# Kernel optimization log

Measured on AMD Instinct MI355X. Metric: run time of the kernel, lower is better.

The kernel has to match this reference:

```python
import jax, jax.numpy as jnp
import numpy as np

N = 50000   # nodes
E = 800000  # edges
G = 128     # graphs in batch
H = 128     # hidden/out dim
K = 3       # GMM kernels
L = 4       # layers
PD = 2      # pseudo_dim_MoNet
NC = 10     # classes
BN_EPS = 1e-5


def setup_inputs() -> dict:
    key = jax.random.key(0)
    ks = jax.random.split(key, 16)
    s = 1.0 / np.sqrt(H)
    inp = {
        "feature": jax.random.normal(ks[0], (N, H), jnp.float32),
        "edge_index": jax.random.randint(ks[1], (2, E), 0, N, dtype=jnp.int32),
        "batch": jnp.sort(jax.random.randint(ks[2], (N,), 0, G, dtype=jnp.int32)),
        "emb_w": jax.random.normal(ks[3], (H, H), jnp.float32) * s,
        "emb_b": jnp.zeros((H,), jnp.float32),
        "fc_w": jax.random.normal(ks[4], (L, K * H, H), jnp.float32) * s,   # per-layer GMMConv fc (no bias)
        "mu": jax.random.normal(ks[5], (L, K, PD), jnp.float32) * 0.1,
        "inv_sigma": jnp.ones((L, K, PD), jnp.float32),
        "bn_gamma": jnp.ones((L, H), jnp.float32),
        "bn_beta": jnp.zeros((L, H), jnp.float32),
        "pp_w": jax.random.normal(ks[6], (L, PD, 2), jnp.float32) * 0.7,   # pseudo_proj Linear(2, dim)
        "pp_b": jnp.zeros((L, PD), jnp.float32),
        "mlp_w0": jax.random.normal(ks[7], (H // 2, H), jnp.float32) * s,
        "mlp_b0": jnp.zeros((H // 2,), jnp.float32),
        "mlp_w1": jax.random.normal(ks[8], (H // 4, H // 2), jnp.float32) * (1.0 / np.sqrt(H // 2)),
        "mlp_b1": jnp.zeros((H // 4,), jnp.float32),
        "mlp_w2": jax.random.normal(ks[9], (NC, H // 4), jnp.float32) * (1.0 / np.sqrt(H // 4)),
        "mlp_b2": jnp.zeros((NC,), jnp.float32),
    }
    return inp


def _forward(feature, edge_index, batch, emb_w, emb_b, fc_w, mu, inv_sigma,
             bn_gamma, bn_beta, pp_w, pp_b, mlp_w0, mlp_b0, mlp_w1, mlp_b1, mlp_w2, mlp_b2):
    row, col = edge_index[0], edge_index[1]
    h = feature @ emb_w.T + emb_b                                   # [N,H]

    # degree-based pseudo coordinates (per edge)
    ones_e = jnp.ones((E,), jnp.float32)
    deg_r = jax.ops.segment_sum(ones_e, row, num_segments=N)
    deg_c = jax.ops.segment_sum(ones_e, col, num_segments=N)
    srcs = 1.0 / jnp.sqrt(deg_r[row] + 1.0)
    dsts = 1.0 / jnp.sqrt(deg_c[col] + 1.0)
    pseudo = jnp.stack([srcs, dsts], axis=-1)                        # [E,2]

    for l in range(L):
        h_in = h
        ps = jnp.tanh(pseudo @ pp_w[l].T + pp_b[l])                  # [E,PD]
        # Gaussian mixture edge weights: exp(-0.5 * sum_d ((ps-mu)^2 * inv_sigma^2))
        diff = ps[:, None, :] - mu[l][None, :, :]                    # [E,K,PD]
        w = jnp.exp(-0.5 * jnp.sum(diff * diff * (inv_sigma[l] ** 2)[None], axis=-1))  # [E,K]
        h_src = h[row]                                               # [E,H] gather
        fcl = fc_w[l].reshape(K, H, H)
        msg = jnp.zeros((E, H), h.dtype)
        for k in range(K):                                           # small fixed K, avoids [E,K,H]
            msg = msg + w[:, k:k + 1] * (h_src @ fcl[k].T)
        agg = jax.ops.segment_sum(msg, col, num_segments=N)          # scatter-add to dst [N,H]
        # batch norm (batch statistics) + ReLU + residual; dropout=0 (identity)
        mean = jnp.mean(agg, axis=0)
        var = jnp.var(agg, axis=0)
        hn = (agg - mean) * jax.lax.rsqrt(var + BN_EPS) * bn_gamma[l] + bn_beta[l]
        h = h_in + jax.nn.relu(hn)

    # mean readout over graphs
    hs = jax.ops.segment_sum(h, batch, num_segments=G)               # [G,H]
    cnt = jax.ops.segment_sum(jnp.ones((N,), jnp.float32), batch, num_segments=G)
    hg = hs / jnp.maximum(cnt, 1.0)[:, None]

    z = jax.nn.relu(hg @ mlp_w0.T + mlp_b0)
    z = jax.nn.relu(z @ mlp_w1.T + mlp_b1)
    return z @ mlp_w2.T + mlp_b2                                     # [G,NC]


def reference(feature, edge_index, batch, emb_w, emb_b, fc_w, mu, inv_sigma,
              bn_gamma, bn_beta, pp_w, pp_b, mlp_w0, mlp_b0, mlp_w1, mlp_b1, mlp_w2, mlp_b2):
    return _forward(feature, edge_index, batch, emb_w, emb_b, fc_w, mu, inv_sigma,
                    bn_gamma, bn_beta, pp_w, pp_b, mlp_w0, mlp_b0, mlp_w1, mlp_b1, mlp_w2, mlp_b2)
```

## Files before the change

### kernel.cpp

```cpp
#include <hip/hip_runtime.h>
#include <hip/hip_bf16.h>

#define N_NODES 50000
#define N_EDGES 800000
#define N_GRAPHS 128
#define HID 128
#define NK 3
#define NL 4
#define NC 10
#define BN_EPS 1e-5f
#define SCAN_G ((N_NODES + 255) / 256)
#define NSLICE 32

#define BKT_SZ 8192
#define NBKT 7
#define FP_CHK 128
#define FP_E (N_EDGES / FP_CHK)

#define H_CHK 64
#define H_E (N_EDGES / H_CHK)
#define PKW (N_NODES / 2)

typedef __attribute__((ext_vector_type(8))) _Float16 half8;
typedef __attribute__((ext_vector_type(4))) float floatx4;
typedef __attribute__((ext_vector_type(2))) float float2v;
typedef __attribute__((ext_vector_type(2))) _Float16 half2v;
typedef __attribute__((ext_vector_type(4))) _Float16 half4v;

__device__ __forceinline__ float tanh_fast(float x) {
    float ax = fabsf(x);
    float t = __expf(-2.0f * ax);
    float r = (1.0f - t) / (1.0f + t);
    return copysignf(r, x);
}

__global__ __launch_bounds__(256) void hist_lds_kernel(const int* __restrict__ row,
                                                       const int* __restrict__ col,
                                                       unsigned* __restrict__ pr,
                                                       unsigned* __restrict__ pc) {
    __shared__ unsigned hh[PKW];
    int tid = threadIdx.x;
    const int4* arr = (const int4*)(blockIdx.y ? col : row);
    unsigned* out = (blockIdx.y ? pc : pr) + (size_t)blockIdx.x * PKW;
    uint4* hh4 = (uint4*)hh;
    const uint4 z4 = {0u, 0u, 0u, 0u};
    for (int i = tid; i < PKW / 4; i += 256) hh4[i] = z4;
    __syncthreads();
    int base4 = blockIdx.x * (H_E / 4);
    for (int i = tid; i < H_E / 4; i += 256) {
        int4 v = arr[base4 + i];
        atomicAdd(&hh[v.x >> 1], 1u << ((v.x & 1) << 4));
        atomicAdd(&hh[v.y >> 1], 1u << ((v.y & 1) << 4));
        atomicAdd(&hh[v.z >> 1], 1u << ((v.z & 1) << 4));
        atomicAdd(&hh[v.w >> 1], 1u << ((v.w & 1) << 4));
    }
    __syncthreads();
    uint4* out4 = (uint4*)out;
    for (int i = tid; i < PKW / 4; i += 256) out4[i] = hh4[i];
}

__global__ __launch_bounds__(256) void hist_reduce_kernel(const unsigned* __restrict__ pr,
                                                          const unsigned* __restrict__ pc,
                                                          int* __restrict__ degr,
                                                          int* __restrict__ degc) {
    int w = blockIdx.x * 256 + threadIdx.x;
    if (w >= PKW) return;
    unsigned rlo = 0, rhi = 0, clo = 0, chi = 0;
    for (int ch = 0; ch < H_CHK; ++ch) {
        unsigned a = pr[(size_t)ch * PKW + w];
        unsigned b = pc[(size_t)ch * PKW + w];
        rlo += a & 0xFFFFu; rhi += a >> 16;
        clo += b & 0xFFFFu; chi += b >> 16;
    }
    ((int2*)degr)[w] = make_int2((int)rlo, (int)rhi);
    ((int2*)degc)[w] = make_int2((int)clo, (int)chi);
}

__global__ __launch_bounds__(256) void scan1_kernel(const int* __restrict__ degc,
                                                    int* __restrict__ csr_off,
                                                    int* __restrict__ blocksum) {
    __shared__ int buf[256];
    int tid = threadIdx.x;
    int i = blockIdx.x * 256 + tid;
    int v = (i < N_NODES) ? degc[i] : 0;
    buf[tid] = v;
    __syncthreads();
    for (int d = 1; d < 256; d <<= 1) {
        int t = (tid >= d) ? buf[tid - d] : 0;
        __syncthreads();
        buf[tid] += t;
        __syncthreads();
    }
    if (i < N_NODES) csr_off[i] = buf[tid] - v;
    if (tid == 255) blocksum[blockIdx.x] = buf[255];
}

__global__ __launch_bounds__(256) void scan2_kernel(int* __restrict__ blocksum) {
    __shared__ int buf[256];
    int tid = threadIdx.x;
    int v = (tid < SCAN_G) ? blocksum[tid] : 0;
    buf[tid] = v;
    __syncthreads();
    for (int d = 1; d < 256; d <<= 1) {
        int t = (tid >= d) ? buf[tid - d] : 0;
        __syncthreads();
        buf[tid] += t;
        __syncthreads();
    }
    if (tid < SCAN_G) blocksum[tid] = buf[tid] - v;
}

__global__ __launch_bounds__(256) void scan3_kernel(const int* __restrict__ blocksum,
                                                    int* __restrict__ csr_off,
                                                    int* __restrict__ cursor) {
    int i = blockIdx.x * 256 + threadIdx.x;
    if (i < N_NODES) {
        int v = csr_off[i] + blocksum[blockIdx.x];
        csr_off[i] = v;
        cursor[i] = v;
    }
    if (i == 0) csr_off[N_NODES] = N_EDGES;
}

__global__ __launch_bounds__(256) void fill_perm_kernel(const int* __restrict__ col,
                                                        int* __restrict__ cursor,
                                                        int* __restrict__ perm) {
    int bkt = blockIdx.x & 7;
    if (bkt >= NBKT) return;
    int chunk = blockIdx.x >> 3;
    int base = bkt * BKT_SZ;
    int e0 = chunk * FP_E;
    for (int e = e0 + threadIdx.x; e < e0 + FP_E; e += 256) {
        unsigned c = (unsigned)(col[e] - base);
        if (c < BKT_SZ) {
            int pos = atomicAdd(&cursor[base + (int)c], 1);
            perm[pos] = e;
        }
    }
}

__global__ void edge_w_rec_kernel(const int* __restrict__ perm,
                                  const int* __restrict__ row, const int* __restrict__ col,
                                  const int* __restrict__ degr, const int* __restrict__ degc,
                                  const float* __restrict__ pp_w, const float* __restrict__ pp_b,
                                  const float* __restrict__ mu, const float* __restrict__ isig,
                                  int4* __restrict__ wrec) {
    int pos = blockIdx.x * blockDim.x + threadIdx.x;
    if (pos >= N_EDGES) return;
    int e = perm[pos];
    int r = row[e], c = col[e];
    float px = rsqrtf((float)degr[r] + 1.0f);
    float py = rsqrtf((float)degc[c] + 1.0f);
    int roff = r << 8;
#pragma unroll
    for (int l = 0; l < NL; ++l) {
        float ps0 = tanh_fast(px * pp_w[l * 4 + 0] + py * pp_w[l * 4 + 1] + pp_b[l * 2 + 0]);
        float ps1 = tanh_fast(px * pp_w[l * 4 + 2] + py * pp_w[l * 4 + 3] + pp_b[l * 2 + 1]);
        float w[NK];
#pragma unroll
        for (int k = 0; k < NK; ++k) {
            float d0 = ps0 - mu[l * 6 + k * 2 + 0], d1 = ps1 - mu[l * 6 + k * 2 + 1];
            float s0 = isig[l * 6 + k * 2 + 0],     s1 = isig[l * 6 + k * 2 + 1];
            w[k] = __expf(-0.5f * (d0 * d0 * s0 * s0 + d1 * d1 * s1 * s1));
        }
        wrec[(size_t)l * N_EDGES + pos] =
            make_int4(roff, __float_as_int(w[0]), __float_as_int(w[1]), __float_as_int(w[2]));
    }
}

__global__ void cvt16_dual_kernel(const float4* __restrict__ a, int n4a,
                                  const float4* __restrict__ b, int n4b,
                                  half4v* __restrict__ da, half4v* __restrict__ db) {
    int i = blockIdx.x * blockDim.x + threadIdx.x;
    const float4* src; half4v* dst; int idx;
    if (i < n4a) { src = a; dst = da; idx = i; }
    else if (i < n4a + n4b) { src = b; dst = db; idx = i - n4a; }
    else return;
    float4 f = src[idx];
    half4v o;
    o.x = (_Float16)f.x; o.y = (_Float16)f.y; o.z = (_Float16)f.z; o.w = (_Float16)f.w;
    dst[idx] = o;
}

__global__ void transpose_fc16_kernel(const float* __restrict__ fc_w,
                                      _Float16* __restrict__ w2t) {
    int idx = blockIdx.x * blockDim.x + threadIdx.x;
    if (idx >= NL * NK * HID * HID) return;
    int i = idx & (HID - 1);
    int j = (idx >> 7) & (HID - 1);
    int kl = idx >> 14;
    int k = kl % 3;
    int l = kl / 3;
    w2t[((size_t)(l * HID + j)) * (NK * HID) + k * HID + i] = (_Float16)fc_w[idx];
}

__global__ __launch_bounds__(256) void gemm_f16_kernel(
        const _Float16* __restrict__ A, const _Float16* __restrict__ W,
        const float* __restrict__ bias, _Float16* __restrict__ C16,
        float* __restrict__ bnsum, int M, int Kd) {
    __shared__ _Float16 sA[128 * 40], sB[128 * 40];
    __shared__ float bsum[HID], bsq[HID];
    int tid = threadIdx.x;
    if (bnsum && tid < HID) { bsum[tid] = 0.f; bsq[tid] = 0.f; }
    int bm = blockIdx.x * 128;
    int wave = tid >> 6, lane = tid & 63;
    int ln = lane & 15, quad = lane >> 4;
    int wy = wave >> 1, wx = wave & 1;
    int srow = tid >> 2, scol = (tid & 3) << 3;
    floatx4 acc[4][4] = {};
    const half8 zv = {0, 0, 0, 0, 0, 0, 0, 0};

    half8 pA[2], pB[2];
    bool av0 = (bm + srow) < M, av1 = (bm + srow + 64) < M;
    const size_t aoff0 = (size_t)(bm + srow) * Kd + scol;
    const size_t aoff1 = (size_t)(bm + srow + 64) * Kd + scol;
    const size_t woff0 = (size_t)srow * Kd + scol;
    const size_t woff1 = (size_t)(srow + 64) * Kd + scol;

#define LOAD_TILE(K0)                                                          \
    do {                                                                       \
        pB[0] = *(const half8*)(W + woff0 + (K0));                             \
        pB[1] = *(const half8*)(W + woff1 + (K0));                             \
        pA[0] = av0 ? *(const half8*)(A + aoff0 + (K0)) : zv;                  \
        pA[1] = av1 ? *(const half8*)(A + aoff1 + (K0)) : zv;                  \
    } while (0)

    LOAD_TILE(0);
    for (int k0 = 0; k0 < Kd; k0 += 32) {
        __syncthreads();
#pragma unroll
        for (int rep = 0; rep < 2; ++rep) {
            int r = srow + rep * 64;
            *(half8*)&sA[r * 40 + scol] = pA[rep];
            *(half8*)&sB[r * 40 + scol] = pB[rep];
        }
        __syncthreads();
        if (k0 + 32 < Kd) LOAD_TILE(k0 + 32);
        half8 a[4], b[4];
        int kq = quad * 8;
#pragma unroll
        for (int i = 0; i < 4; ++i) {
            a[i] = *(const half8*)&sA[(wy * 64 + i * 16 + ln) * 40 + kq];
            b[i] = *(const half8*)&sB[(wx * 64 + i * 16 + ln) * 40 + kq];
        }
#pragma unroll
        for (int i = 0; i < 4; ++i)
#pragma unroll
            for (int j = 0; j < 4; ++j)
                acc[i][j] = __builtin_amdgcn_mfma_f32_16x16x32_f16(a[i], b[j], acc[i][j], 0, 0, 0);
    }
#undef LOAD_TILE

#pragma unroll
    for (int j = 0; j < 4; ++j) {
        int gc = wx * 64 + j * 16 + ln;
        float bv = bias ? bias[gc] : 0.f;
#pragma unroll
        for (int i = 0; i < 4; ++i) {
#pragma unroll
            for (int r = 0; r < 4; ++r) {
                int gr = bm + wy * 64 + i * 16 + quad * 4 + r;
                if (gr < M) C16[(size_t)gr * HID + gc] = (_Float16)(acc[i][j][r] + bv);
            }
        }
    }
    if (bnsum) {
#pragma unroll
        for (int j = 0; j < 4; ++j) {
            float s = 0.f, q = 0.f;
#pragma unroll
            for (int i = 0; i < 4; ++i)
#pragma unroll
                for (int r = 0; r < 4; ++r) { float v = acc[i][j][r]; s += v; q += v * v; }
            s += __shfl_xor(s, 16); s += __shfl_xor(s, 32);
            q += __shfl_xor(q, 16); q += __shfl_xor(q, 32);
            if (quad == 0) {
                atomicAdd(&bsum[wx * 64 + j * 16 + ln], s);
                atomicAdd(&bsq[wx * 64 + j * 16 + ln], q);
            }
        }
        __syncthreads();
        float* slice = bnsum + (blockIdx.x & (NSLICE - 1)) * (2 * HID);
        if (tid < HID) {
            atomicAdd(&slice[tid],       bsum[tid]);
            atomicAdd(&slice[HID + tid], bsq[tid]);
        }
    }
}

__global__ __launch_bounds__(128) void bn_finalize_kernel(const float* __restrict__ slices,
                                                          const float* __restrict__ gamma,
                                                          const float* __restrict__ beta,
                                                          float* __restrict__ sc_sh) {
    int t = threadIdx.x;
    float s = 0.f, q = 0.f;
    for (int sl = 0; sl < NSLICE; ++sl) {
        s += slices[sl * (2 * HID) + t];
        q += slices[sl * (2 * HID) + HID + t];
    }
    const float invN = 1.0f / (float)N_NODES;
    float mean = s * invN;
    float var = q * invN - mean * mean;
    float scale = gamma[t] * rsqrtf(var + BN_EPS);
    sc_sh[t] = scale;
    sc_sh[HID + t] = beta[t] - mean * scale;
}

__global__ __launch_bounds__(256) void aggregate_kernel(const int* __restrict__ csr_off,
                                                        const int4* __restrict__ wrec,
                                                        const char* __restrict__ h16,
                                                        _Float16* __restrict__ u) {
    int wave = threadIdx.x >> 6;
    int lane = threadIdx.x & 63;
    int n = blockIdx.x * 4 + wave;
    if (n >= N_NODES) return;
    int beg = csr_off[n], end = csr_off[n + 1];
    const char* hb = h16 + lane * 4;
    float2v a0 = {0.f, 0.f}, a1 = {0.f, 0.f}, a2 = {0.f, 0.f};
    for (int chunk = beg; chunk < end; chunk += 64) {
        int ce = chunk + lane;
        int roff = 0;
        float w0 = 0.f, w1 = 0.f, w2 = 0.f;
        if (ce < end) {
            int4 md = wrec[ce];
            roff = md.x;
            w0 = __int_as_float(md.y);
            w1 = __int_as_float(md.z);
            w2 = __int_as_float(md.w);
        }
        int m = end - chunk; if (m > 64) m = 64;
        int t = 0;
        for (; t + 16 <= m; t += 16) {
            int ro[16];
#pragma unroll
            for (int s = 0; s < 16; ++s) ro[s] = __shfl(roff, t + s);
            half2v hv[16];
#pragma unroll
            for (int s = 0; s < 16; ++s) hv[s] = *(const half2v*)(hb + (unsigned)ro[s]);
#pragma unroll
            for (int g = 0; g < 4; ++g) {
                float wx[4], wy[4], wz[4];
#pragma unroll
                for (int s = 0; s < 4; ++s) {
                    wx[s] = __shfl(w0, t + g * 4 + s);
                    wy[s] = __shfl(w1, t + g * 4 + s);
                    wz[s] = __shfl(w2, t + g * 4 + s);
                }
#pragma unroll
                for (int s = 0; s < 4; ++s) {
                    half2v hh = hv[g * 4 + s];
                    float2v hf = {(float)hh.x, (float)hh.y};
                    a0 += wx[s] * hf;
                    a1 += wy[s] * hf;
                    a2 += wz[s] * hf;
                }
            }
        }
        for (; t + 8 <= m; t += 8) {
            int ro[8];
#pragma unroll
            for (int s = 0; s < 8; ++s) ro[s] = __shfl(roff, t + s);
            half2v hv[8];
#pragma unroll
            for (int s = 0; s < 8; ++s) hv[s] = *(const half2v*)(hb + (unsigned)ro[s]);
            float wx[8], wy[8], wz[8];
#pragma unroll
            for (int s = 0; s < 8; ++s) {
                wx[s] = __shfl(w0, t + s);
                wy[s] = __shfl(w1, t + s);
                wz[s] = __shfl(w2, t + s);
            }
#pragma unroll
            for (int s = 0; s < 8; ++s) {
                float2v hf = {(float)hv[s].x, (float)hv[s].y};
                a0 += wx[s] * hf;
                a1 += wy[s] * hf;
                a2 += wz[s] * hf;
            }
        }
        for (; t < m; ++t) {
            int ro = __shfl(roff, t);
            float wx = __shfl(w0, t), wy = __shfl(w1, t), wz = __shfl(w2, t);
            half2v hv = *(const half2v*)(hb + (unsigned)ro);
            float2v hf = {(float)hv.x, (float)hv.y};
            a0 += wx * hf;
            a1 += wy * hf;
            a2 += wz * hf;
        }
    }
    size_t base = (size_t)n * 384 + lane * 2;
    half2v o0, o1, o2;
    o0.x = (_Float16)a0.x; o0.y = (_Float16)a0.y;
    o1.x = (_Float16)a1.x; o1.y = (_Float16)a1.y;
    o2.x = (_Float16)a2.x; o2.y = (_Float16)a2.y;
    *(half2v*)(u + base)       = o0;
    *(half2v*)(u + base + 128) = o1;
    *(half2v*)(u + base + 256) = o2;
}

__global__ void bn_apply_kernel(half4v* __restrict__ h16,
                                const half4v* __restrict__ agg16,
                                const float* __restrict__ sc_sh) {
    int idx = blockIdx.x * blockDim.x + threadIdx.x;
    if (idx >= N_NODES * HID / 4) return;
    int c = (idx & 31) * 4;
    half4v a = agg16[idx];
    half4v hv = h16[idx];
    half4v o16;
#pragma unroll
    for (int j = 0; j < 4; ++j) {
        float hn = (float)a[j] * sc_sh[c + j] + sc_sh[HID + c + j];
        o16[j] = (_Float16)((float)hv[j] + fmaxf(hn, 0.f));
    }
    h16[idx] = o16;
}

__global__ __launch_bounds__(128) void readout_mlp_kernel(const _Float16* __restrict__ h16,
                                                          const int* __restrict__ batch,
                                                          const float* __restrict__ w0, const float* __restrict__ b0,
                                                          const float* __restrict__ w1, const float* __restrict__ b1,
                                                          const float* __restrict__ w2, const float* __restrict__ b2,
                                                          float* __restrict__ out) {
    __shared__ float hg[128];
    __shared__ float z0[64];
    __shared__ float z1[32];
    __shared__ int range[2];
    int g = blockIdx.x;
    int tid = threadIdx.x;
    if (tid == 0) {
        int lo = 0, hi = N_NODES;
        while (lo < hi) { int mid = (lo + hi) >> 1; if (batch[mid] < g) lo = mid + 1; else hi = mid; }
        range[0] = lo;
        hi = N_NODES;
        while (lo < hi) { int mid = (lo + hi) >> 1; if (batch[mid] < g + 1) lo = mid + 1; else hi = mid; }
        range[1] = lo;
    }
    __syncthreads();
    int lo = range[0], hi = range[1];
    float s0 = 0.f, s1 = 0.f, s2 = 0.f, s3 = 0.f;
    int n = lo;
    for (; n + 4 <= hi; n += 4) {
        s0 += (float)h16[(size_t)n * HID + tid];
        s1 += (float)h16[(size_t)(n + 1) * HID + tid];
        s2 += (float)h16[(size_t)(n + 2) * HID + tid];
        s3 += (float)h16[(size_t)(n + 3) * HID + tid];
    }
    for (; n < hi; ++n) s0 += (float)h16[(size_t)n * HID + tid];
    float s = (s0 + s1) + (s2 + s3);
    int cnt = hi - lo; if (cnt < 1) cnt = 1;
    hg[tid] = s / (float)cnt;
    __syncthreads();
    if (tid < 64) {
        float a = b0[tid];
        for (int i = 0; i < 128; ++i) a += hg[i] * w0[tid * 128 + i];
        z0[tid] = fmaxf(a, 0.f);
    }
    __syncthreads();
    if (tid < 32) {
        float a = b1[tid];
        for (int i = 0; i < 64; ++i) a += z0[i] * w1[tid * 64 + i];
        z1[tid] = fmaxf(a, 0.f);
    }
    __syncthreads();
    if (tid < 10) {
        float a = b2[tid];
        for (int i = 0; i < 32; ++i) a += z1[i] * w2[tid * 32 + i];
        out[g * NC + tid] = a;
    }
}

extern "C" void kernel_launch(void* const* d_in, const int* in_sizes, int n_in,
                              void* d_out, int out_size, void* d_ws, size_t ws_size,
                              hipStream_t stream) {
    const float* feature = (const float*)d_in[0];
    const int*   edge    = (const int*)d_in[1];
    const int*   row     = edge;
    const int*   col     = edge + N_EDGES;
    const int*   batch   = (const int*)d_in[2];
    const float* emb_w   = (const float*)d_in[3];
    const float* emb_b   = (const float*)d_in[4];
    const float* fc_w    = (const float*)d_in[5];
    const float* mu      = (const float*)d_in[6];
    const float* isig    = (const float*)d_in[7];
    const float* gamma   = (const float*)d_in[8];
    const float* beta    = (const float*)d_in[9];
    const float* pp_w    = (const float*)d_in[10];
    const float* pp_b    = (const float*)d_in[11];
    const float* mw0     = (const float*)d_in[12];
    const float* mb0     = (const float*)d_in[13];
    const float* mw1     = (const float*)d_in[14];
    const float* mb1     = (const float*)d_in[15];
    const float* mw2     = (const float*)d_in[16];
    const float* mb2     = (const float*)d_in[17];
    float* out = (float*)d_out;

    char* ws = (char*)d_ws;
    size_t off = 0;
    auto carve = [&](size_t bytes) { size_t o = off; off = (off + bytes + 255) & ~(size_t)255; return o; };
    _Float16* h16   = (_Float16*)(ws + carve((size_t)N_NODES * HID * 2));
    _Float16* u     = (_Float16*)(ws + carve((size_t)N_NODES * NK * HID * 2));
    _Float16* agg16 = (_Float16*)(ws + carve((size_t)N_NODES * HID * 2));
    int* perm       = (int*)(ws + carve((size_t)N_EDGES * 4));
    int4* wrec      = (int4*)(ws + carve((size_t)NL * N_EDGES * 16));
    _Float16* w2t   = (_Float16*)(ws + carve((size_t)NL * HID * NK * HID * 2));
    _Float16* f16   = (_Float16*)(ws + carve((size_t)N_NODES * HID * 2));
    _Float16* e16   = (_Float16*)(ws + carve((size_t)HID * HID * 2));
    int* degr       = (int*)(ws + carve((size_t)N_NODES * 4));
    int* degc       = (int*)(ws + carve((size_t)N_NODES * 4));
    int* csr_off    = (int*)(ws + carve((size_t)(N_NODES + 1) * 4));
    int* cursor     = (int*)(ws + carve((size_t)N_NODES * 4));
    int* blocksum   = (int*)(ws + carve((size_t)SCAN_G * 4));
    unsigned* pr    = (unsigned*)(ws + carve((size_t)H_CHK * PKW * 4));
    unsigned* pc    = (unsigned*)(ws + carve((size_t)H_CHK * PKW * 4));
    float* bnsum    = (float*)(ws + carve((size_t)NL * NSLICE * 2 * HID * 4));
    float* bnfin    = (float*)(ws + carve((size_t)NL * 2 * HID * 4));
    (void)ws_size; (void)in_sizes; (void)n_in; (void)out_size;

    hipMemsetAsync(bnsum, 0, (size_t)NL * NSLICE * 2 * HID * 4, stream);

    hist_lds_kernel<<<dim3(H_CHK, 2), 256, 0, stream>>>(row, col, pr, pc);
    hist_reduce_kernel<<<(PKW + 255) / 256, 256, 0, stream>>>(pr, pc, degr, degc);
    scan1_kernel<<<SCAN_G, 256, 0, stream>>>(degc, csr_off, blocksum);
    scan2_kernel<<<1, 256, 0, stream>>>(blocksum);
    scan3_kernel<<<SCAN_G, 256, 0, stream>>>(blocksum, csr_off, cursor);
    fill_perm_kernel<<<FP_CHK * 8, 256, 0, stream>>>(col, cursor, perm);
    edge_w_rec_kernel<<<(N_EDGES + 255) / 256, 256, 0, stream>>>(
        perm, row, col, degr, degc, pp_w, pp_b, mu, isig, wrec);

    cvt16_dual_kernel<<<((N_NODES * HID + HID * HID) / 4 + 255) / 256, 256, 0, stream>>>(
        (const float4*)feature, N_NODES * HID / 4, (const float4*)emb_w, HID * HID / 4,
        (half4v*)f16, (half4v*)e16);
    transpose_fc16_kernel<<<(NL * NK * HID * HID + 255) / 256, 256, 0, stream>>>(fc_w, w2t);

    gemm_f16_kernel<<<(N_NODES + 127) / 128, 256, 0, stream>>>(
        f16, e16, emb_b, h16, nullptr, N_NODES, HID);

    for (int l = 0; l < NL; ++l) {
        aggregate_kernel<<<(N_NODES + 3) / 4, 256, 0, stream>>>(
            csr_off, wrec + (size_t)l * N_EDGES, (const char*)h16, u);
        gemm_f16_kernel<<<(N_NODES + 127) / 128, 256, 0, stream>>>(
            u, w2t + (size_t)l * HID * NK * HID, nullptr, agg16,
            bnsum + (size_t)l * NSLICE * 2 * HID, N_NODES, NK * HID);
        bn_finalize_kernel<<<1, 128, 0, stream>>>(
            bnsum + (size_t)l * NSLICE * 2 * HID, gamma + l * HID, beta + l * HID,
            bnfin + l * 2 * HID);
        bn_apply_kernel<<<(N_NODES * HID / 4 + 255) / 256, 256, 0, stream>>>(
            (half4v*)h16, (const half4v*)agg16, bnfin + l * 2 * HID);
    }

    readout_mlp_kernel<<<N_GRAPHS, 128, 0, stream>>>(h16, batch, mw0, mb0, mw1, mb1, mw2, mb2, out);
}
```

Baseline: 529.0 us.

## Balance aggregation across waves with fixed 64-edge windows instead of one node per wave

Replaces the node-per-wave aggregation kernel with an edge-balanced one. A precomputed window table gives each wave a contiguous slice of about 64 CSR-ordered edges, and a new per-edge destination array lets the wave tell where one node ends and the next begins. The wave accumulates per node, flushes the results when the destination changes, and zero-fills nodes that have no incoming edges. This is meant to cut per-node wave overhead and lane underuse on low-degree nodes, at the cost of a per-edge shuffle and branch inside the inner loop, an extra setup kernel, and reuse of the histogram scratch buffers for the new arrays.

Result: slower. 1.307 ms (+147.0%).

```diff
diff --git a/kernel.cpp b/kernel.cpp
--- a/kernel.cpp
+++ b/kernel.cpp
@@ -20,6 +20,9 @@
 #define H_CHK 64
 #define H_E (N_EDGES / H_CHK)
 #define PKW (N_NODES / 2)
+
+#define AG_WIN 64
+#define NWAVE (N_EDGES / AG_WIN)
 
 typedef __attribute__((ext_vector_type(8))) _Float16 half8;
 typedef __attribute__((ext_vector_type(4))) float floatx4;
@@ -120,6 +123,23 @@
         cursor[i] = v;
     }
     if (i == 0) csr_off[N_NODES] = N_EDGES;
+}
+
+__global__ __launch_bounds__(256) void wtab_kernel(const int* __restrict__ csr_off,
+                                                   int2* __restrict__ wtab) {
+    int n = blockIdx.x * 256 + threadIdx.x;
+    if (n > N_NODES) return;
+    if (n == N_NODES) {
+        int w0 = (csr_off[N_NODES - 1] >> 6) + 1;
+        for (int w = w0; w < NWAVE; ++w) wtab[w] = make_int2(N_NODES, N_EDGES);
+        wtab[NWAVE] = make_int2(N_NODES, N_EDGES);
+        return;
+    }
+    int cur = csr_off[n];
+    int w0 = (n == 0) ? 0 : ((csr_off[n - 1] >> 6) + 1);
+    int w1 = cur >> 6;
+    if (w1 > NWAVE - 1) w1 = NWAVE - 1;
+    for (int w = w0; w <= w1; ++w) wtab[w] = make_int2(n, cur);
 }
 
 __global__ __launch_bounds__(256) void fill_perm_kernel(const int* __restrict__ col,
@@ -144,7 +164,7 @@
                                   const int* __restrict__ degr, const int* __restrict__ degc,
                                   const float* __restrict__ pp_w, const float* __restrict__ pp_b,
                                   const float* __restrict__ mu, const float* __restrict__ isig,
-                                  int4* __restrict__ wrec) {
+                                  int4* __restrict__ wrec, int* __restrict__ dstp) {
     int pos = blockIdx.x * blockDim.x + threadIdx.x;
     if (pos >= N_EDGES) return;
     int e = perm[pos];
@@ -152,6 +172,7 @@
     float px = rsqrtf((float)degr[r] + 1.0f);
     float py = rsqrtf((float)degc[c] + 1.0f);
     int roff = r << 8;
+    dstp[pos] = c;
 #pragma unroll
     for (int l = 0; l < NL; ++l) {
         float ps0 = tanh_fast(px * pp_w[l * 4 + 0] + py * pp_w[l * 4 + 1] + pp_b[l * 2 + 0]);
@@ -306,96 +327,99 @@
     sc_sh[HID + t] = beta[t] - mean * scale;
 }
 
-__global__ __launch_bounds__(256) void aggregate_kernel(const int* __restrict__ csr_off,
-                                                        const int4* __restrict__ wrec,
-                                                        const char* __restrict__ h16,
-                                                        _Float16* __restrict__ u) {
-    int wave = threadIdx.x >> 6;
+__global__ __launch_bounds__(256) void aggregate2_kernel(const int2* __restrict__ wtab,
+                                                         const int4* __restrict__ wrec,
+                                                         const int* __restrict__ dstp,
+                                                         const char* __restrict__ h16,
+                                                         _Float16* __restrict__ u) {
+    int wv = blockIdx.x * 4 + (threadIdx.x >> 6);
     int lane = threadIdx.x & 63;
-    int n = blockIdx.x * 4 + wave;
-    if (n >= N_NODES) return;
-    int beg = csr_off[n], end = csr_off[n + 1];
+    int2 ta = wtab[wv];
+    int2 tb = wtab[wv + 1];
+    int n0 = ta.x, beg = ta.y;
+    int n1 = tb.x, end = tb.y;
     const char* hb = h16 + lane * 4;
-    float2v a0 = {0.f, 0.f}, a1 = {0.f, 0.f}, a2 = {0.f, 0.f};
-    for (int chunk = beg; chunk < end; chunk += 64) {
-        int ce = chunk + lane;
-        int roff = 0;
-        float w0 = 0.f, w1 = 0.f, w2 = 0.f;
-        if (ce < end) {
-            int4 md = wrec[ce];
-            roff = md.x;
-            w0 = __int_as_float(md.y);
-            w1 = __int_as_float(md.z);
-            w2 = __int_as_float(md.w);
-        }
-        int m = end - chunk; if (m > 64) m = 64;
-        int t = 0;
-        for (; t + 16 <= m; t += 16) {
+    const float2v z2 = {0.f, 0.f};
+    float2v a0 = z2, a1 = z2, a2 = z2;
+    int cur = -1;
+    int nextn = n0;
+
+    for (int p0 = beg; p0 < end; p0 += 64) {
+        int pl = p0 + lane;
+        int4 md = make_int4(0, 0, 0, 0);
+        int dst = 0;
+        if (pl < end) { md = wrec[pl]; dst = dstp[pl]; }
+        int cnt = end - p0; if (cnt > 64) cnt = 64;
+#pragma unroll
+        for (int g = 0; g < 4; ++g) {
+            int t0 = g * 16;
+            if (t0 >= cnt) break;
             int ro[16];
-#pragma unroll
-            for (int s = 0; s < 16; ++s) ro[s] = __shfl(roff, t + s);
             half2v hv[16];
 #pragma unroll
-            for (int s = 0; s < 16; ++s) hv[s] = *(const half2v*)(hb + (unsigned)ro[s]);
-#pragma unroll
-            for (int g = 0; g < 4; ++g) {
-                float wx[4], wy[4], wz[4];
-#pragma unroll
-                for (int s = 0; s < 4; ++s) {
-                    wx[s] = __shfl(w0, t + g * 4 + s);
-                    wy[s] = __shfl(w1, t + g * 4 + s);
-                    wz[s] = __shfl(w2, t + g * 4 + s);
+            for (int s = 0; s < 16; ++s) {
+                int t = t0 + s;
+                ro[s] = __shfl(md.x, t < cnt ? t : 0);
+            }
+#pragma unroll
+            for (int s = 0; s < 16; ++s)
+                hv[s] = *(const half2v*)(hb + (unsigned)ro[s]);
+#pragma unroll
+            for (int s = 0; s < 16; ++s) {
+                int t = t0 + s;
+                if (t >= cnt) break;
+                int nd = __shfl(dst, t);
+                if (nd != cur) {
+                    if (cur >= 0) {
+                        size_t base = (size_t)cur * 384 + lane * 2;
+                        half2v o0, o1, o2;
+                        o0.x = (_Float16)a0.x; o0.y = (_Float16)a0.y;
+                        o1.x = (_Float16)a1.x; o1.y = (_Float16)a1.y;
+                        o2.x = (_Float16)a2.x; o2.y = (_Float16)a2.y;
+                        *(half2v*)(u + base)       = o0;
+                        *(half2v*)(u + base + 128) = o1;
+                        *(half2v*)(u + base + 256) = o2;
+                        a0 = z2; a1 = z2; a2 = z2;
+                    }
+                    while (nextn < nd) {
+                        size_t base = (size_t)nextn * 384 + lane * 2;
+                        half2v oz; oz.x = (_Float16)0.f; oz.y = (_Float16)0.f;
+                        *(half2v*)(u + base)       = oz;
+                        *(half2v*)(u + base + 128) = oz;
+                        *(half2v*)(u + base + 256) = oz;
+                        ++nextn;
+                    }
+                    cur = nd;
+                    nextn = nd + 1;
                 }
-#pragma unroll
-                for (int s = 0; s < 4; ++s) {
-                    half2v hh = hv[g * 4 + s];
-                    float2v hf = {(float)hh.x, (float)hh.y};
-                    a0 += wx[s] * hf;
-                    a1 += wy[s] * hf;
-                    a2 += wz[s] * hf;
-                }
+                float wx = __int_as_float(__shfl(md.y, t));
+                float wy = __int_as_float(__shfl(md.z, t));
+                float wz = __int_as_float(__shfl(md.w, t));
+                float2v hf = {(float)hv[s].x, (float)hv[s].y};
+                a0 += wx * hf;
+                a1 += wy * hf;
+                a2 += wz * hf;
             }
         }
-        for (; t + 8 <= m; t += 8) {
-            int ro[8];
-#pragma unroll
-            for (int s = 0; s < 8; ++s) ro[s] = __shfl(roff, t + s);
-            half2v hv[8];
-#pragma unroll
-            for (int s = 0; s < 8; ++s) hv[s] = *(const half2v*)(hb + (unsigned)ro[s]);
-            float wx[8], wy[8], wz[8];
-#pragma unroll
-            for (int s = 0; s < 8; ++s) {
-                wx[s] = __shfl(w0, t + s);
-                wy[s] = __shfl(w1, t + s);
-                wz[s] = __shfl(w2, t + s);
-            }
-#pragma unroll
-            for (int s = 0; s < 8; ++s) {
-                float2v hf = {(float)hv[s].x, (float)hv[s].y};
-                a0 += wx[s] * hf;
-                a1 += wy[s] * hf;
-                a2 += wz[s] * hf;
-            }
-        }
-        for (; t < m; ++t) {
-            int ro = __shfl(roff, t);
-            float wx = __shfl(w0, t), wy = __shfl(w1, t), wz = __shfl(w2, t);
-            half2v hv = *(const half2v*)(hb + (unsigned)ro);
-            float2v hf = {(float)hv.x, (float)hv.y};
-            a0 += wx * hf;
-            a1 += wy * hf;
-            a2 += wz * hf;
-        }
-    }
-    size_t base = (size_t)n * 384 + lane * 2;
-    half2v o0, o1, o2;
-    o0.x = (_Float16)a0.x; o0.y = (_Float16)a0.y;
-    o1.x = (_Float16)a1.x; o1.y = (_Float16)a1.y;
-    o2.x = (_Float16)a2.x; o2.y = (_Float16)a2.y;
-    *(half2v*)(u + base)       = o0;
-    *(half2v*)(u + base + 128) = o1;
-    *(half2v*)(u + base + 256) = o2;
+    }
+    if (cur >= 0) {
+        size_t base = (size_t)cur * 384 + lane * 2;
+        half2v o0, o1, o2;
+        o0.x = (_Float16)a0.x; o0.y = (_Float16)a0.y;
+        o1.x = (_Float16)a1.x; o1.y = (_Float16)a1.y;
+        o2.x = (_Float16)a2.x; o2.y = (_Float16)a2.y;
+        *(half2v*)(u + base)       = o0;
+        *(half2v*)(u + base + 128) = o1;
+        *(half2v*)(u + base + 256) = o2;
+    }
+    while (nextn < n1) {
+        size_t base = (size_t)nextn * 384 + lane * 2;
+        half2v oz; oz.x = (_Float16)0.f; oz.y = (_Float16)0.f;
+        *(half2v*)(u + base)       = oz;
+        *(half2v*)(u + base + 128) = oz;
+        *(half2v*)(u + base + 256) = oz;
+        ++nextn;
+    }
 }
 
 __global__ void bn_apply_kernel(half4v* __restrict__ h16,
@@ -514,6 +538,8 @@
     unsigned* pc    = (unsigned*)(ws + carve((size_t)H_CHK * PKW * 4));
     float* bnsum    = (float*)(ws + carve((size_t)NL * NSLICE * 2 * HID * 4));
     float* bnfin    = (float*)(ws + carve((size_t)NL * 2 * HID * 4));
+    int* dstp       = (int*)pr;
+    int2* wtab      = (int2*)pc;
     (void)ws_size; (void)in_sizes; (void)n_in; (void)out_size;
 
     hipMemsetAsync(bnsum, 0, (size_t)NL * NSLICE * 2 * HID * 4, stream);
@@ -523,9 +549,10 @@
     scan1_kernel<<<SCAN_G, 256, 0, stream>>>(degc, csr_off, blocksum);
     scan2_kernel<<<1, 256, 0, stream>>>(blocksum);
     scan3_kernel<<<SCAN_G, 256, 0, stream>>>(blocksum, csr_off, cursor);
+    wtab_kernel<<<(N_NODES + 1 + 255) / 256, 256, 0, stream>>>(csr_off, wtab);
     fill_perm_kernel<<<FP_CHK * 8, 256, 0, stream>>>(col, cursor, perm);
     edge_w_rec_kernel<<<(N_EDGES + 255) / 256, 256, 0, stream>>>(
-        perm, row, col, degr, degc, pp_w, pp_b, mu, isig, wrec);
+        perm, row, col, degr, degc, pp_w, pp_b, mu, isig, wrec, dstp);
 
     cvt16_dual_kernel<<<((N_NODES * HID + HID * HID) / 4 + 255) / 256, 256, 0, stream>>>(
         (const float4*)feature, N_NODES * HID / 4, (const float4*)emb_w, HID * HID / 4,
@@ -536,8 +563,8 @@
         f16, e16, emb_b, h16, nullptr, N_NODES, HID);
 
     for (int l = 0; l < NL; ++l) {
-        aggregate_kernel<<<(N_NODES + 3) / 4, 256, 0, stream>>>(
-            csr_off, wrec + (size_t)l * N_EDGES, (const char*)h16, u);
+        aggregate2_kernel<<<NWAVE / 4, 256, 0, stream>>>(
+            wtab, wrec + (size_t)l * N_EDGES, dstp, (const char*)h16, u);
         gemm_f16_kernel<<<(N_NODES + 127) / 128, 256, 0, stream>>>(
             u, w2t + (size_t)l * HID * NK * HID, nullptr, agg16,
             bnsum + (size_t)l * NSLICE * 2 * HID, N_NODES, NK * HID);
```
